# Kernel optimization log

Measured on AMD Instinct MI355X. Metric: run time of the kernel, lower is better.

Reference implementation:

```python
import jax, jax.numpy as jnp
import numpy as np

N = 50000   # nodes
E = 800000  # edges (avg degree 16)
D = 128     # in_dim == out_dim
EPS = 1e-5  # LayerNorm eps (torch default)


def setup_inputs() -> dict:
    key = jax.random.key(0)
    ks = jax.random.split(key, 8)
    x = jax.random.normal(ks[0], (N, D), dtype=jnp.float32)
    edge_row = jax.random.randint(ks[1], (E,), 0, N, dtype=jnp.int32)
    edge_col = jax.random.randint(ks[2], (E,), 0, N, dtype=jnp.int32)
    edge_val = jax.random.uniform(ks[3], (E,), dtype=jnp.float32)
    W = jax.random.normal(ks[4], (D, D), dtype=jnp.float32) / np.sqrt(D).astype(np.float32)
    b = jnp.zeros((D,), jnp.float32)
    gamma = jnp.ones((D,), jnp.float32)
    beta = jnp.zeros((D,), jnp.float32)
    return {"x": x, "edge_val": edge_val, "W": W, "b": b,
            "gamma": gamma, "beta": beta,
            "edge_row": edge_row, "edge_col": edge_col}


def reference(x, edge_val, W, b, gamma, beta, edge_row, edge_col):
    # SpMM: support = adj @ x, adj in COO form (row, col, val)
    msgs = edge_val[:, None] * x[edge_col]                      # [E, D] gather
    support = jax.ops.segment_sum(msgs, edge_row, num_segments=x.shape[0])  # [N, D]
    # Linear (torch stores weight as [out, in])
    h = support @ W.T + b                                       # [N, D]
    # LayerNorm over last dim
    mu = jnp.mean(h, axis=-1, keepdims=True)
    var = jnp.mean(jnp.square(h - mu), axis=-1, keepdims=True)
    h = (h - mu) * jax.lax.rsqrt(var + EPS) * gamma + beta
    # ReLU; dropout is identity at inference
    return jax.nn.relu(h)
```

## Files before the change

kernel.cpp:

```cpp
#include <hip/hip_runtime.h>

#define D 128
#define LN_EPS 1e-5f
#define RPB 16
#define POISON 0xAAAAAAAAu
#define BINSTRIDE 4864
#define XST_STRIDE 68
#define ECAP 68
#define EMAX 64
#define P1BLOCKS 512
#define P1THREADS 1024
#define DENSECAP 1600
#define CURSTRIDE 16

typedef __attribute__((ext_vector_type(8))) short short8;
typedef __attribute__((ext_vector_type(4))) float f32x4;

union FragU { uint4 u; short8 s; };

__device__ __forceinline__ unsigned bf16_hi(float f) {
    unsigned u = __float_as_uint(f);
    return (u + 0x7FFFu + ((u >> 16) & 1u)) & 0xFFFF0000u;
}
__device__ __forceinline__ float lo16f(unsigned u) { return __uint_as_float(u << 16); }
__device__ __forceinline__ float hi16f(unsigned u) { return __uint_as_float(u & 0xFFFF0000u); }

__global__ void __launch_bounds__(P1THREADS) prep1_kernel(
    const int* __restrict__ edge_row, const int* __restrict__ edge_col,
    const float* __restrict__ edge_val,
    const float* __restrict__ W, const float* __restrict__ x,
    unsigned* __restrict__ yb16,
    unsigned* __restrict__ bin_cursor, uint2* __restrict__ binbuf,
    int E, int N, int nbins, int epb) {
    __shared__ unsigned wbL[8192];
    __shared__ unsigned xst[4][RPB][XST_STRIDE];
    __shared__ int cntL[256];
    __shared__ int curL[256];
    __shared__ int lbaseL[256];
    __shared__ int gbaseL[256];
    __shared__ int tmp[2][256];
    __shared__ uint2 dense[DENSECAP];
    int t = threadIdx.x;

    if (t < 256) cntL[t] = 0;

    for (int i = t; i < 8192; i += P1THREADS) {
        int u  = i & 3;
        int L  = (i >> 2) & 63;
        int nt = (i >> 8) & 7;
        int kt = i >> 11;
        int n = nt * 16 + (L & 15);
        int k = kt * 32 + (L >> 4) * 8 + u * 2;
        unsigned lo = bf16_hi(W[n * D + k]) >> 16;
        unsigned hi = bf16_hi(W[n * D + k + 1]);
        wbL[i] = hi | lo;
    }
    __syncthreads();

    {
        int T = (N + RPB - 1) / RPB;
        int g = t >> 8;
        int tg = t & 255;
        for (int tb0 = blockIdx.x * 4; tb0 < T; tb0 += gridDim.x * 4) {
            int tile = tb0 + g;
            if (tile < T) {
                int r = tg >> 4, q = tg & 15;
                int row = tile * RPB + r;
                uint4 o = make_uint4(0u, 0u, 0u, 0u);
                if (row < N) {
                    float4 a = *(const float4*)(x + (size_t)row * D + q * 8);
                    float4 c = *(const float4*)(x + (size_t)row * D + q * 8 + 4);
                    o.x = bf16_hi(a.y) | (bf16_hi(a.x) >> 16);
                    o.y = bf16_hi(a.w) | (bf16_hi(a.z) >> 16);
                    o.z = bf16_hi(c.y) | (bf16_hi(c.x) >> 16);
                    o.w = bf16_hi(c.w) | (bf16_hi(c.z) >> 16);
                }
                *(uint4*)&xst[g][r][q * 4] = o;
            }
            __syncthreads();
            if (tile < T) {
                int L = tg & 63;
                int w = tg >> 6;
                int m = L & 15;
                int gk = L >> 4;
                f32x4 acc0 = {0.f, 0.f, 0.f, 0.f};
                f32x4 acc1 = {0.f, 0.f, 0.f, 0.f};
#pragma unroll
                for (int kt = 0; kt < 4; ++kt) {
                    FragU a, b0, b1;
                    a.u  = *(const uint4*)&xst[g][m][kt * 16 + gk * 4];
                    b0.u = *(const uint4*)(wbL + (((size_t)(kt * 8 + w * 2)) * 64 + L) * 4);
                    b1.u = *(const uint4*)(wbL + (((size_t)(kt * 8 + w * 2 + 1)) * 64 + L) * 4);
                    acc0 = __builtin_amdgcn_mfma_f32_16x16x32_bf16(a.s, b0.s, acc0, 0, 0, 0);
                    acc1 = __builtin_amdgcn_mfma_f32_16x16x32_bf16(a.s, b1.s, acc1, 0, 0, 0);
                }
                bool evenm = (m & 1) == 0;
#pragma unroll
                for (int i = 0; i < 4; ++i) {
                    float p0 = __shfl_xor(acc0[i], 1);
                    float p1 = __shfl_xor(acc1[i], 1);
                    if (evenm) {
                        int row = tile * RPB + gk * 4 + i;
                        if (row < N) {
                            unsigned y0 = bf16_hi(p0) | (bf16_hi(acc0[i]) >> 16);
                            unsigned y1 = bf16_hi(p1) | (bf16_hi(acc1[i]) >> 16);
                            size_t base = (size_t)row * (D / 2) + w * 16 + (m >> 1);
                            yb16[base] = y0;
                            yb16[base + 8] = y1;
                        }
                    }
                }
            }
            __syncthreads();
        }
    }

    int e0 = blockIdx.x * epb;
    int e1 = e0 + epb; if (e1 > E) e1 = E;
    int nume = e1 - e0; if (nume < 0) nume = 0;

    {
        int i = e0 + t * 4;
        for (; i + 3 < e1; i += P1THREADS * 4) {
            int4 r = *(const int4*)(edge_row + i);
            atomicAdd(&cntL[r.x >> 8], 1);
            atomicAdd(&cntL[r.y >> 8], 1);
            atomicAdd(&cntL[r.z >> 8], 1);
            atomicAdd(&cntL[r.w >> 8], 1);
        }
        for (; i < e1; ++i) atomicAdd(&cntL[edge_row[i] >> 8], 1);
    }
    __syncthreads();

    if (t < nbins) {
        int c = cntL[t];
        gbaseL[t] = c ? (int)(atomicAdd(&bin_cursor[t * CURSTRIDE], (unsigned)c) - POISON) : 0;
    }
    if (t < 256) tmp[0][t] = cntL[t];
    __syncthreads();
    int buf = 0;
    for (int off = 1; off < 256; off <<= 1) {
        if (t < 256) {
            int v = tmp[buf][t];
            if (t >= off) v += tmp[buf][t - off];
            tmp[1 - buf][t] = v;
        }
        buf ^= 1;
        __syncthreads();
    }
    if (t < 256) {
        lbaseL[t] = tmp[buf][t] - cntL[t];
        curL[t] = 0;
    }
    __syncthreads();

    {
        int i = e0 + t * 4;
        for (; i + 3 < e1; i += P1THREADS * 4) {
            int4 r = *(const int4*)(edge_row + i);
            int4 c = *(const int4*)(edge_col + i);
            float4 v = *(const float4*)(edge_val + i);
            int b0 = r.x >> 8, b1 = r.y >> 8, b2 = r.z >> 8, b3 = r.w >> 8;
            int p0 = atomicAdd(&curL[b0], 1) + lbaseL[b0];
            int p1 = atomicAdd(&curL[b1], 1) + lbaseL[b1];
            int p2 = atomicAdd(&curL[b2], 1) + lbaseL[b2];
            int p3 = atomicAdd(&curL[b3], 1) + lbaseL[b3];
            dense[p0] = make_uint2(((unsigned)c.x << 16) | (unsigned)(r.x & 255),
                                   bf16_hi(v.x) | (unsigned)b0);
            dense[p1] = make_uint2(((unsigned)c.y << 16) | (unsigned)(r.y & 255),
                                   bf16_hi(v.y) | (unsigned)b1);
            dense[p2] = make_uint2(((unsigned)c.z << 16) | (unsigned)(r.z & 255),
                                   bf16_hi(v.z) | (unsigned)b2);
            dense[p3] = make_uint2(((unsigned)c.w << 16) | (unsigned)(r.w & 255),
                                   bf16_hi(v.w) | (unsigned)b3);
        }
        for (; i < e1; ++i) {
            int r = edge_row[i];
            int bin = r >> 8;
            int p = atomicAdd(&curL[bin], 1) + lbaseL[bin];
            dense[p] = make_uint2(((unsigned)edge_col[i] << 16) | (unsigned)(r & 255),
                                  bf16_hi(edge_val[i]) | (unsigned)bin);
        }
    }
    __syncthreads();

    for (int i = t; i < nume; i += P1THREADS) {
        uint2 rec = dense[i];
        int bin = (int)(rec.y & 255u);
        int pos = gbaseL[bin] + (i - lbaseL[bin]);
        if (pos < BINSTRIDE)
            binbuf[(size_t)bin * BINSTRIDE + pos] =
                make_uint2(rec.x, rec.y & 0xFFFF0000u);
    }
}

__global__ void __launch_bounds__(256) fused_lite(
    const unsigned* __restrict__ yb16, const uint2* __restrict__ binbuf,
    const unsigned* __restrict__ bin_cursor,
    const float* __restrict__ bias, const float* __restrict__ gamma,
    const float* __restrict__ beta, float* __restrict__ out, int N) {
    __shared__ unsigned ecol[RPB][ECAP];
    __shared__ int ecnt[RPB];
    __shared__ int pdeg[RPB];
    int t = threadIdx.x;

    int nwg = (int)gridDim.x;
    int swq = nwg >> 3, swr = nwg & 7;
    int xcd = (int)blockIdx.x & 7;
    int logical = (xcd < swr ? xcd * (swq + 1) : swr * (swq + 1) + (xcd - swr) * swq)
                + ((int)blockIdx.x >> 3);
    int row0 = logical * RPB;
    int bin  = logical >> 4;
    int tb   = (logical & 15) * RPB;

    if (t < RPB) ecnt[t] = 0;
    int sz = (int)(bin_cursor[bin * CURSTRIDE] - POISON);
    if (sz > BINSTRIDE) sz = BINSTRIDE;
    if (sz < 0) sz = 0;
    const uint2* bb = binbuf + (size_t)bin * BINSTRIDE;
    __syncthreads();

    {
        int half = sz >> 1;
        for (int i = t; i < half; i += 256) {
            uint4 two = *(const uint4*)(bb + (size_t)2 * i);
            int rl0 = (int)(two.x & 255u) - tb;
            if ((unsigned)rl0 < RPB) {
                int p = atomicAdd(&ecnt[rl0], 1);
                if (p < EMAX) ecol[rl0][p] = two.y | (two.x >> 16);
            }
            int rl1 = (int)(two.z & 255u) - tb;
            if ((unsigned)rl1 < RPB) {
                int p = atomicAdd(&ecnt[rl1], 1);
                if (p < EMAX) ecol[rl1][p] = two.w | (two.z >> 16);
            }
        }
        if (t == 0 && (sz & 1)) {
            uint2 rec = bb[sz - 1];
            int rl = (int)(rec.x & 255u) - tb;
            if ((unsigned)rl < RPB) {
                int p = atomicAdd(&ecnt[rl], 1);
                if (p < EMAX) ecol[rl][p] = rec.y | (rec.x >> 16);
            }
        }
    }
    __syncthreads();
    if (t < RPB) {
        int c = ecnt[t]; if (c > EMAX) c = EMAX;
        int pe = (c + 3) & ~3;
        for (int k = c; k < pe; ++k) ecol[t][k] = 0;
        pdeg[t] = pe;
    }
    __syncthreads();

    {
        int r = t >> 4;
        int qd = t & 15;
        int row = row0 + r;
        float4 accA = make_float4(0.f, 0.f, 0.f, 0.f);
        float4 accB = make_float4(0.f, 0.f, 0.f, 0.f);
        if (row < N) {
            int pd = pdeg[r];
            const unsigned* yb = yb16 + qd * 4;
            for (int e = 0; e < pd; e += 4) {
                uint4 p = *(const uint4*)&ecol[r][e];
                unsigned c0 = p.x & 0xFFFFu, c1 = p.y & 0xFFFFu;
                unsigned c2 = p.z & 0xFFFFu, c3 = p.w & 0xFFFFu;
                float w0 = __uint_as_float(p.x & 0xFFFF0000u);
                float w1 = __uint_as_float(p.y & 0xFFFF0000u);
                float w2 = __uint_as_float(p.z & 0xFFFF0000u);
                float w3 = __uint_as_float(p.w & 0xFFFF0000u);
                uint4 X0 = *(const uint4*)(yb + (size_t)c0 * (D / 2));
                uint4 X1 = *(const uint4*)(yb + (size_t)c1 * (D / 2));
                uint4 X2 = *(const uint4*)(yb + (size_t)c2 * (D / 2));
                uint4 X3 = *(const uint4*)(yb + (size_t)c3 * (D / 2));
                accA.x = fmaf(w0, lo16f(X0.x), accA.x);
                accA.y = fmaf(w0, hi16f(X0.x), accA.y);
                accA.z = fmaf(w0, lo16f(X0.y), accA.z);
                accA.w = fmaf(w0, hi16f(X0.y), accA.w);
                accB.x = fmaf(w0, lo16f(X0.z), accB.x);
                accB.y = fmaf(w0, hi16f(X0.z), accB.y);
                accB.z = fmaf(w0, lo16f(X0.w), accB.z);
                accB.w = fmaf(w0, hi16f(X0.w), accB.w);
                accA.x = fmaf(w1, lo16f(X1.x), accA.x);
                accA.y = fmaf(w1, hi16f(X1.x), accA.y);
                accA.z = fmaf(w1, lo16f(X1.y), accA.z);
                accA.w = fmaf(w1, hi16f(X1.y), accA.w);
                accB.x = fmaf(w1, lo16f(X1.z), accB.x);
                accB.y = fmaf(w1, hi16f(X1.z), accB.y);
                accB.z = fmaf(w1, lo16f(X1.w), accB.z);
                accB.w = fmaf(w1, hi16f(X1.w), accB.w);
                accA.x = fmaf(w2, lo16f(X2.x), accA.x);
                accA.y = fmaf(w2, hi16f(X2.x), accA.y);
                accA.z = fmaf(w2, lo16f(X2.y), accA.z);
                accA.w = fmaf(w2, hi16f(X2.y), accA.w);
                accB.x = fmaf(w2, lo16f(X2.z), accB.x);
                accB.y = fmaf(w2, hi16f(X2.z), accB.y);
                accB.z = fmaf(w2, lo16f(X2.w), accB.z);
                accB.w = fmaf(w2, hi16f(X2.w), accB.w);
                accA.x = fmaf(w3, lo16f(X3.x), accA.x);
                accA.y = fmaf(w3, hi16f(X3.x), accA.y);
                accA.z = fmaf(w3, lo16f(X3.y), accA.z);
                accA.w = fmaf(w3, hi16f(X3.y), accA.w);
                accB.x = fmaf(w3, lo16f(X3.z), accB.x);
                accB.y = fmaf(w3, hi16f(X3.z), accB.y);
                accB.z = fmaf(w3, lo16f(X3.w), accB.z);
                accB.w = fmaf(w3, hi16f(X3.w), accB.w);
            }
        }
        float4 bA = *(const float4*)(bias + qd * 8);
        float4 bB = *(const float4*)(bias + qd * 8 + 4);
        accA.x += bA.x; accA.y += bA.y; accA.z += bA.z; accA.w += bA.w;
        accB.x += bB.x; accB.y += bB.y; accB.z += bB.z; accB.w += bB.w;

        float sum = accA.x + accA.y + accA.z + accA.w
                  + accB.x + accB.y + accB.z + accB.w;
        float sq = accA.x * accA.x;
        sq = fmaf(accA.y, accA.y, sq);
        sq = fmaf(accA.z, accA.z, sq);
        sq = fmaf(accA.w, accA.w, sq);
        sq = fmaf(accB.x, accB.x, sq);
        sq = fmaf(accB.y, accB.y, sq);
        sq = fmaf(accB.z, accB.z, sq);
        sq = fmaf(accB.w, accB.w, sq);
#pragma unroll
        for (int off = 8; off > 0; off >>= 1) {
            sum += __shfl_xor(sum, off, 16);
            sq  += __shfl_xor(sq, off, 16);
        }
        float mu = sum * (1.0f / D);
        float var = sq * (1.0f / D) - mu * mu;
        float inv = rsqrtf(var + LN_EPS);

        if (row < N) {
            float4 gA = *(const float4*)(gamma + qd * 8);
            float4 gB = *(const float4*)(gamma + qd * 8 + 4);
            float4 eA = *(const float4*)(beta + qd * 8);
            float4 eB = *(const float4*)(beta + qd * 8 + 4);
            float4 oA, oB;
            oA.x = fmaxf((accA.x - mu) * inv * gA.x + eA.x, 0.f);
            oA.y = fmaxf((accA.y - mu) * inv * gA.y + eA.y, 0.f);
            oA.z = fmaxf((accA.z - mu) * inv * gA.z + eA.z, 0.f);
            oA.w = fmaxf((accA.w - mu) * inv * gA.w + eA.w, 0.f);
            oB.x = fmaxf((accB.x - mu) * inv * gB.x + eB.x, 0.f);
            oB.y = fmaxf((accB.y - mu) * inv * gB.y + eB.y, 0.f);
            oB.z = fmaxf((accB.z - mu) * inv * gB.z + eB.z, 0.f);
            oB.w = fmaxf((accB.w - mu) * inv * gB.w + eB.w, 0.f);
            *(float4*)(out + (size_t)row * D + qd * 8) = oA;
            *(float4*)(out + (size_t)row * D + qd * 8 + 4) = oB;
        }
    }
}

extern "C" void kernel_launch(void* const* d_in, const int* in_sizes, int n_in,
                              void* d_out, int out_size, void* d_ws, size_t ws_size,
                              hipStream_t stream) {
    const float* x        = (const float*)d_in[0];
    const float* edge_val = (const float*)d_in[1];
    const float* W        = (const float*)d_in[2];
    const float* b        = (const float*)d_in[3];
    const float* gamma    = (const float*)d_in[4];
    const float* beta     = (const float*)d_in[5];
    const int*   edge_row = (const int*)d_in[6];
    const int*   edge_col = (const int*)d_in[7];

    const int N = in_sizes[0] / D;
    const int E = in_sizes[1];
    const int nbins = (N + 255) >> 8;

    char* ws = (char*)d_ws;
    uint2*    binbuf     = (uint2*)ws;     ws += (size_t)nbins * BINSTRIDE * sizeof(uint2);
    unsigned* yb16       = (unsigned*)ws;  ws += (size_t)N * (D / 2) * sizeof(unsigned);
    unsigned* bin_cursor = (unsigned*)ws;  ws += 256 * CURSTRIDE * sizeof(unsigned);

    int epb = ((E + P1BLOCKS - 1) / P1BLOCKS + 3) & ~3;

    prep1_kernel<<<P1BLOCKS, P1THREADS, 0, stream>>>(edge_row, edge_col, edge_val,
                                                     W, x, yb16, bin_cursor,
                                                     binbuf, E, N, nbins, epb);
    fused_lite<<<(N + RPB - 1) / RPB, 256, 0, stream>>>(
        yb16, binbuf, bin_cursor, b, gamma, beta, (float*)d_out, N);
}
```

Before: 146.0 us.

## Bin edges per 16-row tile so consumers skip filtering coarse bins

Edges are now bucketed by row>>4 into one bin per 16-row consumer block instead of row>>8 bins shared by 16 blocks. Each consumer block reads only its own edges, so it no longer scans and filters a whole 256-row bin. The producer drops the local dense staging buffer and prefix scan and scatters records directly to global memory through per-bin atomics. In exchange, global cursor atomics rise to 4096 bins, writes become more scattered, and the fixed capacity of 384 edges per bin could overflow on skewed inputs. The XCD-aware block remapping is also removed.

```diff
diff --git a/kernel.cpp b/kernel.cpp
--- a/kernel.cpp
+++ b/kernel.cpp
@@ -4,13 +4,13 @@
 #define LN_EPS 1e-5f
 #define RPB 16
 #define POISON 0xAAAAAAAAu
-#define BINSTRIDE 4864
+#define NBF 4096
+#define BSF 384
 #define XST_STRIDE 68
 #define ECAP 68
 #define EMAX 64
 #define P1BLOCKS 512
 #define P1THREADS 1024
-#define DENSECAP 1600
 #define CURSTRIDE 16
 
 typedef __attribute__((ext_vector_type(8))) short short8;
@@ -31,18 +31,14 @@
     const float* __restrict__ W, const float* __restrict__ x,
     unsigned* __restrict__ yb16,
     unsigned* __restrict__ bin_cursor, uint2* __restrict__ binbuf,
-    int E, int N, int nbins, int epb) {
-    __shared__ unsigned wbL[8192];
-    __shared__ unsigned xst[4][RPB][XST_STRIDE];
-    __shared__ int cntL[256];
-    __shared__ int curL[256];
-    __shared__ int lbaseL[256];
-    __shared__ int gbaseL[256];
-    __shared__ int tmp[2][256];
-    __shared__ uint2 dense[DENSECAP];
+    int E, int N, int epb) {
+    __shared__ __align__(16) char arena[50176];
+    unsigned* wbL = (unsigned*)arena;
+    typedef unsigned XstRow[XST_STRIDE];
+    XstRow* xstA = (XstRow*)(arena + 32768);
+    int* cntL   = (int*)arena;
+    int* gbaseL = (int*)(arena + 16384);
     int t = threadIdx.x;
-
-    if (t < 256) cntL[t] = 0;
 
     for (int i = t; i < 8192; i += P1THREADS) {
         int u  = i & 3;
@@ -61,6 +57,7 @@
         int T = (N + RPB - 1) / RPB;
         int g = t >> 8;
         int tg = t & 255;
+        XstRow* xst = xstA + g * RPB;
         for (int tb0 = blockIdx.x * 4; tb0 < T; tb0 += gridDim.x * 4) {
             int tile = tb0 + g;
             if (tile < T) {
@@ -75,7 +72,7 @@
                     o.z = bf16_hi(c.y) | (bf16_hi(c.x) >> 16);
                     o.w = bf16_hi(c.w) | (bf16_hi(c.z) >> 16);
                 }
-                *(uint4*)&xst[g][r][q * 4] = o;
+                *(uint4*)&xst[r][q * 4] = o;
             }
             __syncthreads();
             if (tile < T) {
@@ -88,7 +85,7 @@
 #pragma unroll
                 for (int kt = 0; kt < 4; ++kt) {
                     FragU a, b0, b1;
-                    a.u  = *(const uint4*)&xst[g][m][kt * 16 + gk * 4];
+                    a.u  = *(const uint4*)&xst[m][kt * 16 + gk * 4];
                     b0.u = *(const uint4*)(wbL + (((size_t)(kt * 8 + w * 2)) * 64 + L) * 4);
                     b1.u = *(const uint4*)(wbL + (((size_t)(kt * 8 + w * 2 + 1)) * 64 + L) * 4);
                     acc0 = __builtin_amdgcn_mfma_f32_16x16x32_bf16(a.s, b0.s, acc0, 0, 0, 0);
@@ -117,40 +114,27 @@
 
     int e0 = blockIdx.x * epb;
     int e1 = e0 + epb; if (e1 > E) e1 = E;
-    int nume = e1 - e0; if (nume < 0) nume = 0;
+
+    for (int b = t; b < NBF; b += P1THREADS) cntL[b] = 0;
+    __syncthreads();
 
     {
         int i = e0 + t * 4;
         for (; i + 3 < e1; i += P1THREADS * 4) {
             int4 r = *(const int4*)(edge_row + i);
-            atomicAdd(&cntL[r.x >> 8], 1);
-            atomicAdd(&cntL[r.y >> 8], 1);
-            atomicAdd(&cntL[r.z >> 8], 1);
-            atomicAdd(&cntL[r.w >> 8], 1);
-        }
-        for (; i < e1; ++i) atomicAdd(&cntL[edge_row[i] >> 8], 1);
-    }
-    __syncthreads();
-
-    if (t < nbins) {
-        int c = cntL[t];
-        gbaseL[t] = c ? (int)(atomicAdd(&bin_cursor[t * CURSTRIDE], (unsigned)c) - POISON) : 0;
-    }
-    if (t < 256) tmp[0][t] = cntL[t];
-    __syncthreads();
-    int buf = 0;
-    for (int off = 1; off < 256; off <<= 1) {
-        if (t < 256) {
-            int v = tmp[buf][t];
-            if (t >= off) v += tmp[buf][t - off];
-            tmp[1 - buf][t] = v;
-        }
-        buf ^= 1;
-        __syncthreads();
-    }
-    if (t < 256) {
-        lbaseL[t] = tmp[buf][t] - cntL[t];
-        curL[t] = 0;
+            atomicAdd(&cntL[r.x >> 4], 1);
+            atomicAdd(&cntL[r.y >> 4], 1);
+            atomicAdd(&cntL[r.z >> 4], 1);
+            atomicAdd(&cntL[r.w >> 4], 1);
+        }
+        for (; i < e1; ++i) atomicAdd(&cntL[edge_row[i] >> 4], 1);
+    }
+    __syncthreads();
+
+    for (int b = t; b < NBF; b += P1THREADS) {
+        int c = cntL[b];
+        gbaseL[b] = c ? (int)(atomicAdd(&bin_cursor[b * CURSTRIDE], (unsigned)c) - POISON) : 0;
+        cntL[b] = 0;
     }
     __syncthreads();
 
@@ -160,37 +144,33 @@
             int4 r = *(const int4*)(edge_row + i);
             int4 c = *(const int4*)(edge_col + i);
             float4 v = *(const float4*)(edge_val + i);
-            int b0 = r.x >> 8, b1 = r.y >> 8, b2 = r.z >> 8, b3 = r.w >> 8;
-            int p0 = atomicAdd(&curL[b0], 1) + lbaseL[b0];
-            int p1 = atomicAdd(&curL[b1], 1) + lbaseL[b1];
-            int p2 = atomicAdd(&curL[b2], 1) + lbaseL[b2];
-            int p3 = atomicAdd(&curL[b3], 1) + lbaseL[b3];
-            dense[p0] = make_uint2(((unsigned)c.x << 16) | (unsigned)(r.x & 255),
-                                   bf16_hi(v.x) | (unsigned)b0);
-            dense[p1] = make_uint2(((unsigned)c.y << 16) | (unsigned)(r.y & 255),
-                                   bf16_hi(v.y) | (unsigned)b1);
-            dense[p2] = make_uint2(((unsigned)c.z << 16) | (unsigned)(r.z & 255),
-                                   bf16_hi(v.z) | (unsigned)b2);
-            dense[p3] = make_uint2(((unsigned)c.w << 16) | (unsigned)(r.w & 255),
-                                   bf16_hi(v.w) | (unsigned)b3);
+            int b0 = r.x >> 4, b1 = r.y >> 4, b2 = r.z >> 4, b3 = r.w >> 4;
+            int p0 = atomicAdd(&cntL[b0], 1) + gbaseL[b0];
+            int p1 = atomicAdd(&cntL[b1], 1) + gbaseL[b1];
+            int p2 = atomicAdd(&cntL[b2], 1) + gbaseL[b2];
+            int p3 = atomicAdd(&cntL[b3], 1) + gbaseL[b3];
+            if (p0 < BSF)
+                binbuf[(size_t)b0 * BSF + p0] =
+                    make_uint2(((unsigned)c.x << 16) | (unsigned)(r.x & 15), bf16_hi(v.x));
+            if (p1 < BSF)
+                binbuf[(size_t)b1 * BSF + p1] =
+                    make_uint2(((unsigned)c.y << 16) | (unsigned)(r.y & 15), bf16_hi(v.y));
+            if (p2 < BSF)
+                binbuf[(size_t)b2 * BSF + p2] =
+                    make_uint2(((unsigned)c.z << 16) | (unsigned)(r.z & 15), bf16_hi(v.z));
+            if (p3 < BSF)
+                binbuf[(size_t)b3 * BSF + p3] =
+                    make_uint2(((unsigned)c.w << 16) | (unsigned)(r.w & 15), bf16_hi(v.w));
         }
         for (; i < e1; ++i) {
             int r = edge_row[i];
-            int bin = r >> 8;
-            int p = atomicAdd(&curL[bin], 1) + lbaseL[bin];
-            dense[p] = make_uint2(((unsigned)edge_col[i] << 16) | (unsigned)(r & 255),
-                                  bf16_hi(edge_val[i]) | (unsigned)bin);
-        }
-    }
-    __syncthreads();
-
-    for (int i = t; i < nume; i += P1THREADS) {
-        uint2 rec = dense[i];
-        int bin = (int)(rec.y & 255u);
-        int pos = gbaseL[bin] + (i - lbaseL[bin]);
-        if (pos < BINSTRIDE)
-            binbuf[(size_t)bin * BINSTRIDE + pos] =
-                make_uint2(rec.x, rec.y & 0xFFFF0000u);
+            int bin = r >> 4;
+            int p = atomicAdd(&cntL[bin], 1) + gbaseL[bin];
+            if (p < BSF)
+                binbuf[(size_t)bin * BSF + p] =
+                    make_uint2(((unsigned)edge_col[i] << 16) | (unsigned)(r & 15),
+                               bf16_hi(edge_val[i]));
+        }
     }
 }
 
@@ -203,46 +183,21 @@
     __shared__ int ecnt[RPB];
     __shared__ int pdeg[RPB];
     int t = threadIdx.x;
-
-    int nwg = (int)gridDim.x;
-    int swq = nwg >> 3, swr = nwg & 7;
-    int xcd = (int)blockIdx.x & 7;
-    int logical = (xcd < swr ? xcd * (swq + 1) : swr * (swq + 1) + (xcd - swr) * swq)
-                + ((int)blockIdx.x >> 3);
-    int row0 = logical * RPB;
-    int bin  = logical >> 4;
-    int tb   = (logical & 15) * RPB;
+    int bin = blockIdx.x;
+    int row0 = bin * RPB;
 
     if (t < RPB) ecnt[t] = 0;
     int sz = (int)(bin_cursor[bin * CURSTRIDE] - POISON);
-    if (sz > BINSTRIDE) sz = BINSTRIDE;
+    if (sz > BSF) sz = BSF;
     if (sz < 0) sz = 0;
-    const uint2* bb = binbuf + (size_t)bin * BINSTRIDE;
-    __syncthreads();
-
-    {
-        int half = sz >> 1;
-        for (int i = t; i < half; i += 256) {
-            uint4 two = *(const uint4*)(bb + (size_t)2 * i);
-            int rl0 = (int)(two.x & 255u) - tb;
-            if ((unsigned)rl0 < RPB) {
-                int p = atomicAdd(&ecnt[rl0], 1);
-                if (p < EMAX) ecol[rl0][p] = two.y | (two.x >> 16);
-            }
-            int rl1 = (int)(two.z & 255u) - tb;
-            if ((unsigned)rl1 < RPB) {
-                int p = atomicAdd(&ecnt[rl1], 1);
-                if (p < EMAX) ecol[rl1][p] = two.w | (two.z >> 16);
-            }
-        }
-        if (t == 0 && (sz & 1)) {
-            uint2 rec = bb[sz - 1];
-            int rl = (int)(rec.x & 255u) - tb;
-            if ((unsigned)rl < RPB) {
-                int p = atomicAdd(&ecnt[rl], 1);
-                if (p < EMAX) ecol[rl][p] = rec.y | (rec.x >> 16);
-            }
-        }
+    const uint2* bb = binbuf + (size_t)bin * BSF;
+    __syncthreads();
+
+    for (int i = t; i < sz; i += 256) {
+        uint2 rec = bb[i];
+        int rl = (int)(rec.x & 15u);
+        int p = atomicAdd(&ecnt[rl], 1);
+        if (p < EMAX) ecol[rl][p] = rec.y | (rec.x >> 16);
     }
     __syncthreads();
     if (t < RPB) {
@@ -366,18 +321,18 @@
 
     const int N = in_sizes[0] / D;
     const int E = in_sizes[1];
-    const int nbins = (N + 255) >> 8;
+    const int nbf = (N + RPB - 1) / RPB;
 
     char* ws = (char*)d_ws;
-    uint2*    binbuf     = (uint2*)ws;     ws += (size_t)nbins * BINSTRIDE * sizeof(uint2);
+    uint2*    binbuf     = (uint2*)ws;     ws += (size_t)nbf * BSF * sizeof(uint2);
     unsigned* yb16       = (unsigned*)ws;  ws += (size_t)N * (D / 2) * sizeof(unsigned);
-    unsigned* bin_cursor = (unsigned*)ws;  ws += 256 * CURSTRIDE * sizeof(unsigned);
+    unsigned* bin_cursor = (unsigned*)ws;  ws += (size_t)NBF * CURSTRIDE * sizeof(unsigned);
 
     int epb = ((E + P1BLOCKS - 1) / P1BLOCKS + 3) & ~3;
 
     prep1_kernel<<<P1BLOCKS, P1THREADS, 0, stream>>>(edge_row, edge_col, edge_val,
                                                      W, x, yb16, bin_cursor,
-                                                     binbuf, E, N, nbins, epb);
-    fused_lite<<<(N + RPB - 1) / RPB, 256, 0, stream>>>(
+                                                     binbuf, E, N, epb);
+    fused_lite<<<nbf, 256, 0, stream>>>(
         yb16, binbuf, bin_cursor, b, gamma, beta, (float*)d_out, N);
 }
```

Result: slower. 170.7 us (+16.9%).
